# Optimization experiments

Hardware: AMD Instinct MI355X
Metric: run time of the kernel (lower is better)

The kernel has to match this reference:

```python
import jax, jax.numpy as jnp
import numpy as np

B, C, H, W, N, NH, DFF = 2, 256, 128, 128, 8, 8, 1024
EPS = 1e-5


def _ln(x, g, b):
    m = jnp.mean(x, -1, keepdims=True)
    v = jnp.mean((x - m) ** 2, -1, keepdims=True)
    return (x - m) / jnp.sqrt(v + EPS) * g + b


def _mha(q, k, v, Wqkv, bqkv, Wo, bo, nh):
    # q,k,v: [Bq, S, C]; torch MultiheadAttention with packed in_proj
    Bq, S, Cd = q.shape
    dh = Cd // nh
    Wq, Wk, Wv = jnp.split(Wqkv, 3, axis=0)
    bq, bk, bv = jnp.split(bqkv, 3, axis=0)
    qp = (q @ Wq.T + bq).reshape(Bq, S, nh, dh).transpose(0, 2, 1, 3)
    kp = (k @ Wk.T + bk).reshape(Bq, S, nh, dh).transpose(0, 2, 1, 3)
    vp = (v @ Wv.T + bv).reshape(Bq, S, nh, dh).transpose(0, 2, 1, 3)
    scores = jnp.einsum('bhqd,bhkd->bhqk', qp, kp) / jnp.sqrt(jnp.asarray(dh, qp.dtype))
    attn = jax.nn.softmax(scores, axis=-1)
    o = jnp.einsum('bhqk,bhkd->bhqd', attn, vp).transpose(0, 2, 1, 3).reshape(Bq, S, Cd)
    return o @ Wo.T + bo


def _enc_layer(q, k, v, Wqkv, bqkv, Wo, bo, W1, b1, W2, b2, g1, be1, g2, be2, nh):
    # normalize_before=False, dropout=0
    src = _ln(v + _mha(q, k, v, Wqkv, bqkv, Wo, bo, nh), g1, be1)
    ffn = jax.nn.relu(src @ W1.T + b1) @ W2.T + b2
    return _ln(src + ffn, g2, be2)


def _encode(feat, pe, layer_params, nh):
    # feat: [Nv, hw, C]; pe = glob_pos + rel_pos broadcast: [Nv, hw, C]
    out = feat
    qk = out + pe
    out = _enc_layer(qk, qk, out, *layer_params, nh)
    out_t = out.transpose(1, 0, 2)                 # [hw, Nv, C] axis-permuted pass
    qk = out_t + pe.transpose(1, 0, 2)
    out = _enc_layer(qk, qk, out_t, *layer_params, nh).transpose(1, 0, 2)
    return out


def _forward(backbone_memory, defe_feature_filtered, glob_pos_embed,
             Wqkv, bqkv, Wo, bo, W1, b1, W2, b2, g1, be1, g2, be2,
             relW1, relb1, relW2, relb2, n):
    Bm, Cd, Hf, Wf = backbone_memory.shape
    h, w = Hf // n, Wf // n
    Nv, hw = n * n, h * w

    # relative position embedding: MLP over normalized grid coords [h,w,2]
    gy, gx = jnp.meshgrid(jnp.arange(h, dtype=jnp.float32),
                          jnp.arange(w, dtype=jnp.float32), indexing='ij')
    coords = jnp.stack([gx / (w - 1), gy / (h - 1)], axis=-1)
    rel = (jax.nn.relu(coords @ relW1.T + relb1) @ relW2.T + relb2)  # [h,w,C]
    rel = rel.reshape(1, hw, Cd)                                      # [1,hw,C]

    # window partition: [B, Nv, hw, C]
    win = backbone_memory.reshape(Bm, Cd, n, h, n, w).transpose(0, 2, 4, 1, 3, 5)
    win = win.reshape(Bm, Nv, Cd, hw).transpose(0, 1, 3, 2)

    # per-window global pos embed: [Nv, hw, C]
    glob = glob_pos_embed.reshape(Cd, n, h, n, w).transpose(1, 3, 0, 2, 4)
    glob = glob.reshape(Nv, Cd, hw).transpose(0, 2, 1)

    pe = glob + rel
    layer_params = (Wqkv, bqkv, Wo, bo, W1, b1, W2, b2, g1, be1, g2, be2)
    enc = jax.vmap(lambda f: _encode(f, pe, layer_params, NH))(win)   # [B,Nv,hw,C]

    # scatter windows back and add residually (reconstructed += feats)
    back = enc.transpose(0, 1, 3, 2).reshape(Bm, n, n, Cd, h, w)
    back = back.transpose(0, 3, 1, 4, 2, 5).reshape(Bm, Cd, Hf, Wf)
    reconstructed = backbone_memory + back

    # defe_mask via non-overlapping max-pool (all-ones mask -> all valid)
    Hm, Wm = defe_feature_filtered.shape[-2:]
    kh = (Hm // Hf) * h
    kw = (Wm // Wf) * w
    pooled = defe_feature_filtered.reshape(Bm, 1, n, kh, n, kw).max(axis=(3, 5))
    defe_mask = pooled[:, 0] > 0
    return reconstructed, defe_mask


def setup_inputs() -> dict:
    key = jax.random.key(0)
    ks = jax.random.split(key, 10)
    s = 0.02
    return {
        'backbone_memory': jax.random.normal(ks[0], (B, C, H, W), jnp.float32),
        'defe_feature_filtered': jnp.ones((B, 1, H, W), jnp.float32),
        'glob_pos_embed': jax.random.normal(ks[1], (C, H, W), jnp.float32),
        'Wqkv': jax.random.normal(ks[2], (3 * C, C), jnp.float32) * s,
        'bqkv': jnp.zeros((3 * C,), jnp.float32),
        'Wo': jax.random.normal(ks[3], (C, C), jnp.float32) * s,
        'bo': jnp.zeros((C,), jnp.float32),
        'W1': jax.random.normal(ks[4], (DFF, C), jnp.float32) * s,
        'b1': jnp.zeros((DFF,), jnp.float32),
        'W2': jax.random.normal(ks[5], (C, DFF), jnp.float32) * s,
        'b2': jnp.zeros((C,), jnp.float32),
        'g1': jnp.ones((C,), jnp.float32),
        'be1': jnp.zeros((C,), jnp.float32),
        'g2': jnp.ones((C,), jnp.float32),
        'be2': jnp.zeros((C,), jnp.float32),
        'relW1': jax.random.normal(ks[6], (64, 2), jnp.float32) * s,
        'relb1': jnp.zeros((64,), jnp.float32),
        'relW2': jax.random.normal(ks[7], (C, 64), jnp.float32) * s,
        'relb2': jnp.zeros((C,), jnp.float32),
        'n': N,
    }


def reference(backbone_memory, defe_feature_filtered, glob_pos_embed,
              Wqkv, bqkv, Wo, bo, W1, b1, W2, b2, g1, be1, g2, be2,
              relW1, relb1, relW2, relb2, n):
    return _forward(backbone_memory, defe_feature_filtered, glob_pos_embed,
                    Wqkv, bqkv, Wo, bo, W1, b1, W2, b2, g1, be1, g2, be2,
                    relW1, relb1, relW2, relb2, n)
```

## Files before the change

### kernel.cpp

```cpp
#include <hip/hip_runtime.h>
#include <hip/hip_bf16.h>

#define C_DIM 256
#define NHEAD 8
#define DH 32
#define NTOK 32768
#define PETOK 16384
#define DFF_DIM 1024
#define LN_EPS 1e-5f

typedef unsigned int u32;
typedef unsigned short ushortT;
using frag_ab = __attribute__((ext_vector_type(8))) short;
using f32x4   = __attribute__((ext_vector_type(4))) float;

__device__ __forceinline__ float bflo(u32 u) { union { u32 i; float f; } c; c.i = u << 16; return c.f; }
__device__ __forceinline__ float bfhi(u32 u) { union { u32 i; float f; } c; c.i = u & 0xffff0000u; return c.f; }
__device__ __forceinline__ ushortT f2b(float f) {
    __hip_bfloat16 b = __float2bfloat16(f);
    return *reinterpret_cast<ushortT*>(&b);
}
__device__ __forceinline__ u32 packbf(float lo, float hi) {
    return (u32)f2b(lo) | ((u32)f2b(hi) << 16);
}
__device__ __forceinline__ void gload_lds16(const ushortT* g, ushortT* l) {
    __builtin_amdgcn_global_load_lds((const __attribute__((address_space(1))) void*)g,
                                     (__attribute__((address_space(3))) void*)l, 16, 0, 0);
}

__global__ void cvt_all_kernel(const float* __restrict__ Wqkv, const float* __restrict__ Wo,
                               const float* __restrict__ W1, const float* __restrict__ W2,
                               ushortT* __restrict__ dst) {
    const int i = (blockIdx.x * 256 + threadIdx.x) * 4;
    const float* src;
    int off;
    if (i < 196608)      { src = Wqkv; off = 0; }
    else if (i < 262144) { src = Wo;   off = 196608; }
    else if (i < 524288) { src = W1;   off = 262144; }
    else                 { src = W2;   off = 524288; }
    const float4 v = *(const float4*)&src[i - off];
    uint2 o = {packbf(v.x, v.y), packbf(v.z, v.w)};
    *(uint2*)&dst[i] = o;
}

__global__ void rel_kernel(const float* __restrict__ relW1, const float* __restrict__ relb1,
                           const float* __restrict__ relW2, const float* __restrict__ relb2,
                           float* __restrict__ rel) {
    __shared__ float hid[64];
    int t = blockIdx.x;
    int ty = t >> 4, tx = t & 15;
    float cx = tx * (1.0f / 15.0f);
    float cy = ty * (1.0f / 15.0f);
    int c = threadIdx.x;
    if (c < 64) {
        float h = relW1[c * 2 + 0] * cx + relW1[c * 2 + 1] * cy + relb1[c];
        hid[c] = fmaxf(h, 0.0f);
    }
    __syncthreads();
    float acc = relb2[c];
    #pragma unroll
    for (int jj = 0; jj < 64; ++jj) acc = fmaf(hid[jj], relW2[c * 64 + jj], acc);
    rel[t * C_DIM + c] = acc;
}

__global__ __launch_bounds__(256) void pe_kernel(const float* __restrict__ glob,
                                                 const float* __restrict__ rel,
                                                 ushortT* __restrict__ peb) {
    __shared__ float tile[32][129];
    const int y = blockIdx.x;
    const int c0 = blockIdx.y * 32;
    const int i = y >> 4, ty = y & 15;
    const int tid = threadIdx.x;
    const int xl = tid & 127;
    #pragma unroll
    for (int p = 0; p < 16; ++p) {
        const int cl = p * 2 + (tid >> 7);
        tile[cl][xl] = glob[(size_t)(c0 + cl) * 16384 + y * 128 + xl];
    }
    __syncthreads();
    const int cl = tid & 31;
    #pragma unroll
    for (int p = 0; p < 16; ++p) {
        const int x = p * 8 + (tid >> 5);
        const int v = i * 8 + (x >> 4);
        const int t = ty * 16 + (x & 15);
        const float val = tile[cl][x] + rel[t * C_DIM + c0 + cl];
        peb[(size_t)(v * 256 + t) * C_DIM + c0 + cl] = f2b(val);
    }
}

__global__ __launch_bounds__(256) void window_kernel(const float* __restrict__ backbone,
                                                     float* __restrict__ Xf, ushortT* __restrict__ Xb) {
    __shared__ float tile[32][129];
    const int y = blockIdx.x;
    const int c0 = blockIdx.y * 32;
    const int b = blockIdx.z;
    const int i = y >> 4, ty = y & 15;
    const int tid = threadIdx.x;
    const int xl = tid & 127;
    #pragma unroll
    for (int p = 0; p < 16; ++p) {
        const int cl = p * 2 + (tid >> 7);
        tile[cl][xl] = backbone[(size_t)b * 4194304 + (size_t)(c0 + cl) * 16384 + y * 128 + xl];
    }
    __syncthreads();
    const int cl = tid & 31;
    #pragma unroll
    for (int p = 0; p < 16; ++p) {
        const int x = p * 8 + (tid >> 5);
        const int v = i * 8 + (x >> 4);
        const int t = ty * 16 + (x & 15);
        const size_t tok = (size_t)b * PETOK + v * 256 + t;
        const float val = tile[cl][x];
        Xf[tok * C_DIM + c0 + cl] = val;
        Xb[tok * C_DIM + c0 + cl] = f2b(val);
    }
}

__global__ __launch_bounds__(256) void scatter_kernel(const float* __restrict__ backbone,
                                                      const float* __restrict__ X,
                                                      float* __restrict__ out) {
    __shared__ float tile[128][33];
    const int y = blockIdx.x;
    const int c0 = blockIdx.y * 32;
    const int b = blockIdx.z;
    const int i = y >> 4, ty = y & 15;
    const int tid = threadIdx.x;
    const int cl = tid & 31;
    #pragma unroll
    for (int p = 0; p < 16; ++p) {
        const int x = p * 8 + (tid >> 5);
        const int v = i * 8 + (x >> 4);
        const int t = ty * 16 + (x & 15);
        const size_t tok = (size_t)b * PETOK + v * 256 + t;
        tile[x][cl] = X[tok * C_DIM + c0 + cl];
    }
    __syncthreads();
    const int xl = tid & 127;
    #pragma unroll
    for (int p = 0; p < 16; ++p) {
        const int c = c0 + p * 2 + (tid >> 7);
        const size_t gi = (size_t)b * 4194304 + (size_t)c * 16384 + y * 128 + xl;
        out[gi] = backbone[gi] + tile[xl][p * 2 + (tid >> 7)];
    }
}

#define BM 128
#define BN 128
#define BK 32

template<bool FUSE_PE, bool RELU>
__global__ __launch_bounds__(256) void gemm_bf16(
        const ushortT* __restrict__ A, int lda,
        const ushortT* __restrict__ peb,
        const ushortT* __restrict__ W,
        const float* __restrict__ bias,
        ushortT* __restrict__ Cout, int ldc, int K) {
    __shared__ ushortT As[BM][BK];
    __shared__ ushortT Bs[BN][BK];
    const int m0 = blockIdx.y * BM;
    const int n0 = blockIdx.x * BN;
    const int tid = threadIdx.x;
    const int lane = tid & 63;
    const int wave = tid >> 6;
    const int wm = (wave >> 1) * 64;
    const int wn = (wave & 1) * 64;
    const int fr = lane & 15;
    const int fg = lane >> 4;
    const int gRow = wave * 32 + (lane >> 2);
    const int gCol = (lane & 3) * 8;
    const int sRow = tid >> 2;
    const int sCol = (tid & 3) * 8;

    f32x4 acc[4][4];
    #pragma unroll
    for (int i = 0; i < 4; ++i)
        #pragma unroll
        for (int j = 0; j < 4; ++j)
            acc[i][j] = (f32x4){0.f, 0.f, 0.f, 0.f};

    for (int k0 = 0; k0 < K; k0 += BK) {
        if (FUSE_PE) {
            #pragma unroll
            for (int h = 0; h < 2; ++h) {
                const int row = sRow + h * 64;
                uint4 av = *(const uint4*)&A[(size_t)(m0 + row) * lda + k0 + sCol];
                const uint4 pv = *(const uint4*)&peb[(size_t)((m0 + row) & 16383) * C_DIM + k0 + sCol];
                u32* a = (u32*)&av;
                const u32* p = (const u32*)&pv;
                #pragma unroll
                for (int e = 0; e < 4; ++e)
                    a[e] = packbf(bflo(a[e]) + bflo(p[e]), bfhi(a[e]) + bfhi(p[e]));
                *(uint4*)&As[row][sCol] = av;
            }
        } else {
            gload_lds16(&A[(size_t)(m0 + gRow) * lda + k0 + gCol], &As[wave * 32][0]);
            gload_lds16(&A[(size_t)(m0 + gRow + 16) * lda + k0 + gCol], &As[wave * 32 + 16][0]);
        }
        gload_lds16(&W[(size_t)(n0 + gRow) * K + k0 + gCol], &Bs[wave * 32][0]);
        gload_lds16(&W[(size_t)(n0 + gRow + 16) * K + k0 + gCol], &Bs[wave * 32 + 16][0]);
        __syncthreads();
        frag_ab af[4], bf[4];
        #pragma unroll
        for (int i = 0; i < 4; ++i) af[i] = *(const frag_ab*)&As[wm + i * 16 + fr][fg * 8];
        #pragma unroll
        for (int j = 0; j < 4; ++j) bf[j] = *(const frag_ab*)&Bs[wn + j * 16 + fr][fg * 8];
        #pragma unroll
        for (int i = 0; i < 4; ++i)
            #pragma unroll
            for (int j = 0; j < 4; ++j)
                acc[i][j] = __builtin_amdgcn_mfma_f32_16x16x32_bf16(af[i], bf[j], acc[i][j], 0, 0, 0);
        __syncthreads();
    }
    #pragma unroll
    for (int j = 0; j < 4; ++j) {
        const float bv = bias[n0 + wn + j * 16 + fr];
        #pragma unroll
        for (int i = 0; i < 4; ++i) {
            #pragma unroll
            for (int r = 0; r < 4; ++r) {
                float v = acc[i][j][r] + bv;
                if (RELU) v = fmaxf(v, 0.0f);
                const int m = m0 + wm + i * 16 + fg * 4 + r;
                const int n = n0 + wn + j * 16 + fr;
                Cout[(size_t)m * ldc + n] = f2b(v);
            }
        }
    }
}

#define KVC 128
__global__ __launch_bounds__(256) void attn_p0(const ushortT* __restrict__ QKb,
                                               const ushortT* __restrict__ Vb,
                                               ushortT* __restrict__ Ob) {
    __shared__ ushortT K_lds[KVC * 40];
    __shared__ ushortT V_t[32 * 136];
    __shared__ ushortT P_lds[4][16 * 136];
    const int grp = blockIdx.x;
    const int h = grp & 7;
    const int bv = grp >> 3;
    const int base = (bv >> 6) * PETOK + (bv & 63) * 256;
    const int tid = threadIdx.x;
    const int wave = tid >> 6;
    const int lane = tid & 63;
    const int fr = lane & 15;
    const int fg = lane >> 4;
    const float scale = 0.17677669529663687f;

    frag_ab qf[4];
    size_t qtok[4];
    #pragma unroll
    for (int s = 0; s < 4; ++s) {
        qtok[s] = (size_t)(base + wave * 64 + s * 16 + fr);
        qf[s] = *(const frag_ab*)&QKb[qtok[s] * 512 + h * DH + fg * 8];
    }
    float m[4], l[4];
    f32x4 o0[4], o1[4];
    #pragma unroll
    for (int s = 0; s < 4; ++s) {
        m[s] = -1e30f; l[s] = 0.f;
        o0[s] = (f32x4){0.f, 0.f, 0.f, 0.f};
        o1[s] = (f32x4){0.f, 0.f, 0.f, 0.f};
    }

    for (int c = 0; c < 2; ++c) {
        __syncthreads();
        #pragma unroll
        for (int it = 0; it < 2; ++it) {
            const int idx = it * 256 + tid;
            const int row = idx >> 2, ch = idx & 3;
            const size_t tok = (size_t)(base + c * KVC + row);
            const uint4 kv = *(const uint4*)&QKb[tok * 512 + 256 + h * DH + ch * 8];
            *(uint4*)&K_lds[row * 40 + ch * 8] = kv;
            const uint4 vv = *(const uint4*)&Vb[tok * C_DIM + h * DH + ch * 8];
            const ushortT* vp = (const ushortT*)&vv;
            #pragma unroll
            for (int e = 0; e < 8; ++e) V_t[(ch * 8 + e) * 136 + row] = vp[e];
        }
        __syncthreads();
        #pragma unroll
        for (int s = 0; s < 4; ++s) {
            f32x4 sc[8];
            #pragma unroll
            for (int kt = 0; kt < 8; ++kt) {
                const frag_ab kf = *(const frag_ab*)&K_lds[(kt * 16 + fr) * 40 + fg * 8];
                sc[kt] = __builtin_amdgcn_mfma_f32_16x16x32_bf16(kf, qf[s], (f32x4){0.f, 0.f, 0.f, 0.f}, 0, 0, 0);
            }
            float mx = -1e30f;
            #pragma unroll
            for (int kt = 0; kt < 8; ++kt)
                mx = fmaxf(mx, fmaxf(fmaxf(sc[kt][0], sc[kt][1]), fmaxf(sc[kt][2], sc[kt][3])));
            mx = fmaxf(mx, __shfl_xor(mx, 16, 64));
            mx = fmaxf(mx, __shfl_xor(mx, 32, 64));
            const float nm = fmaxf(m[s], mx);
            const float corr = __expf((m[s] - nm) * scale);
            m[s] = nm;
            float lsum = 0.f;
            #pragma unroll
            for (int kt = 0; kt < 8; ++kt) {
                const float p0 = __expf((sc[kt][0] - nm) * scale);
                const float p1 = __expf((sc[kt][1] - nm) * scale);
                const float p2 = __expf((sc[kt][2] - nm) * scale);
                const float p3 = __expf((sc[kt][3] - nm) * scale);
                lsum += (p0 + p1) + (p2 + p3);
                uint2 pk;
                pk.x = packbf(p0, p1);
                pk.y = packbf(p2, p3);
                *(uint2*)&P_lds[wave][fr * 136 + kt * 16 + fg * 4] = pk;
            }
            lsum += __shfl_xor(lsum, 16, 64);
            lsum += __shfl_xor(lsum, 32, 64);
            l[s] = l[s] * corr + lsum;
            o0[s] *= corr;
            o1[s] *= corr;
            #pragma unroll
            for (int kc = 0; kc < 4; ++kc) {
                const frag_ab pf = *(const frag_ab*)&P_lds[wave][fr * 136 + kc * 32 + fg * 8];
                const frag_ab v0 = *(const frag_ab*)&V_t[fr * 136 + kc * 32 + fg * 8];
                const frag_ab v1 = *(const frag_ab*)&V_t[(16 + fr) * 136 + kc * 32 + fg * 8];
                o0[s] = __builtin_amdgcn_mfma_f32_16x16x32_bf16(v0, pf, o0[s], 0, 0, 0);
                o1[s] = __builtin_amdgcn_mfma_f32_16x16x32_bf16(v1, pf, o1[s], 0, 0, 0);
            }
        }
    }
    #pragma unroll
    for (int s = 0; s < 4; ++s) {
        const float inv = 1.0f / l[s];
        ushortT* ob = &Ob[qtok[s] * C_DIM + h * DH];
        uint2 w0, w1;
        w0.x = packbf(o0[s][0] * inv, o0[s][1] * inv);
        w0.y = packbf(o0[s][2] * inv, o0[s][3] * inv);
        w1.x = packbf(o1[s][0] * inv, o1[s][1] * inv);
        w1.y = packbf(o1[s][2] * inv, o1[s][3] * inv);
        *(uint2*)&ob[fg * 4] = w0;
        *(uint2*)&ob[16 + fg * 4] = w1;
    }
}

template<int S, int LDK, int LDV, int LDP>
__device__ __forceinline__ void attn_wave_work(
        const ushortT* __restrict__ QKb, ushortT* __restrict__ Ob,
        const ushortT* __restrict__ K_lds, const ushortT* __restrict__ V_t,
        ushortT* __restrict__ P_lds,
        int base, int seqStride, int head, int q0base) {
    constexpr int NKT = S / 16;
    constexpr int NKC = S / 32;
    const int lane = threadIdx.x & 63;
    const int fr = lane & 15;
    const int fg = lane >> 4;
    const float scale = 0.17677669529663687f;
    #pragma unroll
    for (int s = 0; s < 4; ++s) {
        const int qq = q0base + s * 16 + fr;
        const size_t qtok = (size_t)(base + qq * seqStride);
        const frag_ab qf = *(const frag_ab*)&QKb[qtok * 512 + head * DH + fg * 8];
        f32x4 sc[NKT];
        #pragma unroll
        for (int kt = 0; kt < NKT; ++kt) {
            const frag_ab kf = *(const frag_ab*)&K_lds[(kt * 16 + fr) * LDK + fg * 8];
            sc[kt] = __builtin_amdgcn_mfma_f32_16x16x32_bf16(kf, qf, (f32x4){0.f, 0.f, 0.f, 0.f}, 0, 0, 0);
        }
        float mx = -1e30f;
        #pragma unroll
        for (int kt = 0; kt < NKT; ++kt)
            mx = fmaxf(mx, fmaxf(fmaxf(sc[kt][0], sc[kt][1]), fmaxf(sc[kt][2], sc[kt][3])));
        mx = fmaxf(mx, __shfl_xor(mx, 16, 64));
        mx = fmaxf(mx, __shfl_xor(mx, 32, 64));
        float lsum = 0.f;
        #pragma unroll
        for (int kt = 0; kt < NKT; ++kt) {
            const float p0 = __expf((sc[kt][0] - mx) * scale);
            const float p1 = __expf((sc[kt][1] - mx) * scale);
            const float p2 = __expf((sc[kt][2] - mx) * scale);
            const float p3 = __expf((sc[kt][3] - mx) * scale);
            lsum += (p0 + p1) + (p2 + p3);
            uint2 pk;
            pk.x = packbf(p0, p1);
            pk.y = packbf(p2, p3);
            *(uint2*)&P_lds[fr * LDP + kt * 16 + fg * 4] = pk;
        }
        lsum += __shfl_xor(lsum, 16, 64);
        lsum += __shfl_xor(lsum, 32, 64);
        f32x4 o0 = {0.f, 0.f, 0.f, 0.f}, o1 = {0.f, 0.f, 0.f, 0.f};
        #pragma unroll
        for (int kc = 0; kc < NKC; ++kc) {
            const frag_ab pf = *(const frag_ab*)&P_lds[fr * LDP + kc * 32 + fg * 8];
            const frag_ab v0 = *(const frag_ab*)&V_t[fr * LDV + kc * 32 + fg * 8];
            const frag_ab v1 = *(const frag_ab*)&V_t[(16 + fr) * LDV + kc * 32 + fg * 8];
            o0 = __builtin_amdgcn_mfma_f32_16x16x32_bf16(v0, pf, o0, 0, 0, 0);
            o1 = __builtin_amdgcn_mfma_f32_16x16x32_bf16(v1, pf, o1, 0, 0, 0);
        }
        const float inv = 1.0f / lsum;
        ushortT* ob = &Ob[qtok * C_DIM + head * DH];
        uint2 w0, w1;
        w0.x = packbf(o0[0] * inv, o0[1] * inv);
        w0.y = packbf(o0[2] * inv, o0[3] * inv);
        w1.x = packbf(o1[0] * inv, o1[1] * inv);
        w1.y = packbf(o1[2] * inv, o1[3] * inv);
        *(uint2*)&ob[fg * 4] = w0;
        *(uint2*)&ob[16 + fg * 4] = w1;
    }
}

__global__ __launch_bounds__(256) void attn_p1(const ushortT* __restrict__ QKb,
                                               const ushortT* __restrict__ Vb,
                                               ushortT* __restrict__ Ob) {
    __shared__ ushortT K_lds[4][64 * 40];
    __shared__ ushortT V_t[4][32 * 72];
    __shared__ ushortT P_lds[4][16 * 72];
    const int wave = threadIdx.x >> 6;
    const int lane = threadIdx.x & 63;
    const int unit = blockIdx.x * 4 + wave;
    const int h = unit & 7;
    const int g = unit >> 3;
    const int base = (g >> 8) * PETOK + (g & 255);
    #pragma unroll
    for (int it = 0; it < 4; ++it) {
        const int idx = it * 64 + lane;
        const int row = idx >> 2, ch = idx & 3;
        const size_t tok = (size_t)(base + row * 256);
        const uint4 kv = *(const uint4*)&QKb[tok * 512 + 256 + h * DH + ch * 8];
        *(uint4*)&K_lds[wave][row * 40 + ch * 8] = kv;
        const uint4 vv = *(const uint4*)&Vb[tok * C_DIM + h * DH + ch * 8];
        const ushortT* vp = (const ushortT*)&vv;
        #pragma unroll
        for (int e = 0; e < 8; ++e) V_t[wave][(ch * 8 + e) * 72 + row] = vp[e];
    }
    attn_wave_work<64, 40, 72, 72>(QKb, Ob, K_lds[wave], V_t[wave], P_lds[wave], base, 256, h, 0);
}

__global__ __launch_bounds__(256) void ln_kernel(float* __restrict__ X, const ushortT* __restrict__ Y,
                                                 const float* __restrict__ g, const float* __restrict__ be,
                                                 ushortT* __restrict__ Xb) {
    int tok = blockIdx.x * 4 + (threadIdx.x >> 6);
    int lane = threadIdx.x & 63;
    float4 x = *(float4*)&X[(size_t)tok * C_DIM + lane * 4];
    const uint2 yu = *(const uint2*)&Y[(size_t)tok * C_DIM + lane * 4];
    float v0 = x.x + bflo(yu.x), v1 = x.y + bfhi(yu.x);
    float v2 = x.z + bflo(yu.y), v3 = x.w + bfhi(yu.y);
    float s = v0 + v1 + v2 + v3;
    float ss = v0 * v0 + v1 * v1 + v2 * v2 + v3 * v3;
    #pragma unroll
    for (int off = 32; off; off >>= 1) {
        s += __shfl_xor(s, off, 64);
        ss += __shfl_xor(ss, off, 64);
    }
    float mean = s * (1.0f / 256.0f);
    float var = ss * (1.0f / 256.0f) - mean * mean;
    float inv = rsqrtf(var + LN_EPS);
    const float4 gv = *(const float4*)&g[lane * 4];
    const float4 bv = *(const float4*)&be[lane * 4];
    float o0 = (v0 - mean) * inv * gv.x + bv.x;
    float o1 = (v1 - mean) * inv * gv.y + bv.y;
    float o2 = (v2 - mean) * inv * gv.z + bv.z;
    float o3 = (v3 - mean) * inv * gv.w + bv.w;
    float4 of = {o0, o1, o2, o3};
    *(float4*)&X[(size_t)tok * C_DIM + lane * 4] = of;
    uint2 ob = {packbf(o0, o1), packbf(o2, o3)};
    *(uint2*)&Xb[(size_t)tok * C_DIM + lane * 4] = ob;
}

__global__ void mask_kernel(const float* __restrict__ defe, float* __restrict__ out) {
    __shared__ float wmax[4];
    const int idx = blockIdx.x;
    const int b = idx >> 6;
    const int ii = (idx >> 3) & 7;
    const int jj = idx & 7;
    const int t = threadIdx.x;
    const int y = t >> 4, xx = t & 15;
    float v = defe[b * 16384 + (ii * 16 + y) * 128 + jj * 16 + xx];
    #pragma unroll
    for (int off = 32; off; off >>= 1) v = fmaxf(v, __shfl_xor(v, off, 64));
    if ((t & 63) == 0) wmax[t >> 6] = v;
    __syncthreads();
    if (t == 0) {
        float mx = fmaxf(fmaxf(wmax[0], wmax[1]), fmaxf(wmax[2], wmax[3]));
        out[8388608 + idx] = (mx > 0.0f) ? 1.0f : 0.0f;
    }
}

extern "C" void kernel_launch(void* const* d_in, const int* in_sizes, int n_in,
                              void* d_out, int out_size, void* d_ws, size_t ws_size,
                              hipStream_t stream) {
    const float* backbone = (const float*)d_in[0];
    const float* defe     = (const float*)d_in[1];
    const float* glob     = (const float*)d_in[2];
    const float* Wqkv     = (const float*)d_in[3];
    const float* bqkv     = (const float*)d_in[4];
    const float* Wo       = (const float*)d_in[5];
    const float* bo       = (const float*)d_in[6];
    const float* W1       = (const float*)d_in[7];
    const float* b1       = (const float*)d_in[8];
    const float* W2       = (const float*)d_in[9];
    const float* b2       = (const float*)d_in[10];
    const float* g1       = (const float*)d_in[11];
    const float* be1      = (const float*)d_in[12];
    const float* g2       = (const float*)d_in[13];
    const float* be2      = (const float*)d_in[14];
    const float* relW1    = (const float*)d_in[15];
    const float* relb1    = (const float*)d_in[16];
    const float* relW2    = (const float*)d_in[17];
    const float* relb2    = (const float*)d_in[18];

    ushortT* peb    = (ushortT*)d_ws;
    ushortT* Wqkv_b = peb + 4194304;
    ushortT* Wo_b   = Wqkv_b + 196608;
    ushortT* W1_b   = Wo_b + 65536;
    ushortT* W2_b   = W1_b + 262144;
    ushortT* Xb     = W2_b + 262144;
    ushortT* QKb    = Xb + 8388608;
    ushortT* Vb     = QKb + 16777216;
    ushortT* Ob     = Vb + 8388608;
    ushortT* Hb     = QKb;
    ushortT* Yb     = Ob + 8388608;
    float*   Xf     = (float*)(Yb + 8388608);
    float*   relf   = Xf + 8388608;
    size_t needed = (size_t)((char*)(relf + 65536) - (char*)d_ws);
    if (ws_size < needed) return;

    cvt_all_kernel<<<768, 256, 0, stream>>>(Wqkv, Wo, W1, W2, Wqkv_b);
    rel_kernel<<<256, 256, 0, stream>>>(relW1, relb1, relW2, relb2, relf);
    pe_kernel<<<dim3(128, 8), 256, 0, stream>>>(glob, relf, peb);
    window_kernel<<<dim3(128, 8, 2), 256, 0, stream>>>(backbone, Xf, Xb);

    for (int pass = 0; pass < 2; ++pass) {
        gemm_bf16<true, false><<<dim3(512 / BN, NTOK / BM), 256, 0, stream>>>(
            Xb, C_DIM, peb, Wqkv_b, bqkv, QKb, 512, C_DIM);
        gemm_bf16<false, false><<<dim3(256 / BN, NTOK / BM), 256, 0, stream>>>(
            Xb, C_DIM, nullptr, Wqkv_b + 512 * 256, bqkv + 512, Vb, C_DIM, C_DIM);
        if (pass == 0) {
            attn_p0<<<128 * NHEAD, 256, 0, stream>>>(QKb, Vb, Ob);
        } else {
            attn_p1<<<4096 / 4, 256, 0, stream>>>(QKb, Vb, Ob);
        }
        gemm_bf16<false, false><<<dim3(256 / BN, NTOK / BM), 256, 0, stream>>>(
            Ob, C_DIM, nullptr, Wo_b, bo, Yb, C_DIM, C_DIM);
        ln_kernel<<<NTOK / 4, 256, 0, stream>>>(Xf, Yb, g1, be1, Xb);
        gemm_bf16<false, true><<<dim3(DFF_DIM / BN, NTOK / BM), 256, 0, stream>>>(
            Xb, C_DIM, nullptr, W1_b, b1, Hb, DFF_DIM, C_DIM);
        gemm_bf16<false, false><<<dim3(256 / BN, NTOK / BM), 256, 0, stream>>>(
            Hb, DFF_DIM, nullptr, W2_b, b2, Yb, C_DIM, DFF_DIM);
        ln_kernel<<<NTOK / 4, 256, 0, stream>>>(Xf, Yb, g2, be2, Xb);
    }

    scatter_kernel<<<dim3(128, 8, 2), 256, 0, stream>>>(backbone, Xf, (float*)d_out);
    mask_kernel<<<128, 256, 0, stream>>>(defe, (float*)d_out);
}
```

Baseline: 411.3 us.

## Double-buffer GEMM LDS tiles, drop fp32 residual copy, skew V transpose stores

The GEMM kernel now double-buffers its A/B LDS tiles, prefetching the next K slice (via registers for the PE-fused path) while MFMAs run on the current slice, and needs one barrier per iteration instead of two. The fp32 residual stream Xf is removed: LayerNorm, windowing and scatter read and write only the bf16 copy, which cuts memory traffic but stores the residual at lower precision. The V transpose stores in both attention kernels are rotated per chunk to reduce LDS bank conflicts.

```diff
diff --git a/kernel.cpp b/kernel.cpp
--- a/kernel.cpp
+++ b/kernel.cpp
@@ -16,6 +16,7 @@
 
 __device__ __forceinline__ float bflo(u32 u) { union { u32 i; float f; } c; c.i = u << 16; return c.f; }
 __device__ __forceinline__ float bfhi(u32 u) { union { u32 i; float f; } c; c.i = u & 0xffff0000u; return c.f; }
+__device__ __forceinline__ float b2f(ushortT u) { union { u32 i; float f; } c; c.i = ((u32)u) << 16; return c.f; }
 __device__ __forceinline__ ushortT f2b(float f) {
     __hip_bfloat16 b = __float2bfloat16(f);
     return *reinterpret_cast<ushortT*>(&b);
@@ -90,7 +91,7 @@
 }
 
 __global__ __launch_bounds__(256) void window_kernel(const float* __restrict__ backbone,
-                                                     float* __restrict__ Xf, ushortT* __restrict__ Xb) {
+                                                     ushortT* __restrict__ Xb) {
     __shared__ float tile[32][129];
     const int y = blockIdx.x;
     const int c0 = blockIdx.y * 32;
@@ -111,16 +112,14 @@
         const int v = i * 8 + (x >> 4);
         const int t = ty * 16 + (x & 15);
         const size_t tok = (size_t)b * PETOK + v * 256 + t;
-        const float val = tile[cl][x];
-        Xf[tok * C_DIM + c0 + cl] = val;
-        Xb[tok * C_DIM + c0 + cl] = f2b(val);
+        Xb[tok * C_DIM + c0 + cl] = f2b(tile[cl][x]);
     }
 }
 
 __global__ __launch_bounds__(256) void scatter_kernel(const float* __restrict__ backbone,
-                                                      const float* __restrict__ X,
+                                                      const ushortT* __restrict__ X,
                                                       float* __restrict__ out) {
-    __shared__ float tile[128][33];
+    __shared__ ushortT tile[128][34];
     const int y = blockIdx.x;
     const int c0 = blockIdx.y * 32;
     const int b = blockIdx.z;
@@ -141,7 +140,7 @@
     for (int p = 0; p < 16; ++p) {
         const int c = c0 + p * 2 + (tid >> 7);
         const size_t gi = (size_t)b * 4194304 + (size_t)c * 16384 + y * 128 + xl;
-        out[gi] = backbone[gi] + tile[xl][p * 2 + (tid >> 7)];
+        out[gi] = backbone[gi] + b2f(tile[xl][p * 2 + (tid >> 7)]);
     }
 }
 
@@ -156,8 +155,8 @@
         const ushortT* __restrict__ W,
         const float* __restrict__ bias,
         ushortT* __restrict__ Cout, int ldc, int K) {
-    __shared__ ushortT As[BM][BK];
-    __shared__ ushortT Bs[BN][BK];
+    __shared__ ushortT As[2][BM][BK];
+    __shared__ ushortT Bs[2][BN][BK];
     const int m0 = blockIdx.y * BM;
     const int n0 = blockIdx.x * BN;
     const int tid = threadIdx.x;
@@ -171,6 +170,7 @@
     const int gCol = (lane & 3) * 8;
     const int sRow = tid >> 2;
     const int sCol = (tid & 3) * 8;
+    const int nk = K / BK;
 
     f32x4 acc[4][4];
     #pragma unroll
@@ -179,38 +179,77 @@
         for (int j = 0; j < 4; ++j)
             acc[i][j] = (f32x4){0.f, 0.f, 0.f, 0.f};
 
-    for (int k0 = 0; k0 < K; k0 += BK) {
-        if (FUSE_PE) {
-            #pragma unroll
-            for (int h = 0; h < 2; ++h) {
-                const int row = sRow + h * 64;
-                uint4 av = *(const uint4*)&A[(size_t)(m0 + row) * lda + k0 + sCol];
-                const uint4 pv = *(const uint4*)&peb[(size_t)((m0 + row) & 16383) * C_DIM + k0 + sCol];
-                u32* a = (u32*)&av;
-                const u32* p = (const u32*)&pv;
-                #pragma unroll
-                for (int e = 0; e < 4; ++e)
-                    a[e] = packbf(bflo(a[e]) + bflo(p[e]), bfhi(a[e]) + bfhi(p[e]));
-                *(uint4*)&As[row][sCol] = av;
-            }
-        } else {
-            gload_lds16(&A[(size_t)(m0 + gRow) * lda + k0 + gCol], &As[wave * 32][0]);
-            gload_lds16(&A[(size_t)(m0 + gRow + 16) * lda + k0 + gCol], &As[wave * 32 + 16][0]);
-        }
-        gload_lds16(&W[(size_t)(n0 + gRow) * K + k0 + gCol], &Bs[wave * 32][0]);
-        gload_lds16(&W[(size_t)(n0 + gRow + 16) * K + k0 + gCol], &Bs[wave * 32 + 16][0]);
-        __syncthreads();
+    uint4 avr0, avr1, pvr0, pvr1;
+    if (FUSE_PE) {
+        avr0 = *(const uint4*)&A[(size_t)(m0 + sRow) * lda + sCol];
+        pvr0 = *(const uint4*)&peb[(size_t)((m0 + sRow) & 16383) * C_DIM + sCol];
+        avr1 = *(const uint4*)&A[(size_t)(m0 + sRow + 64) * lda + sCol];
+        pvr1 = *(const uint4*)&peb[(size_t)((m0 + sRow + 64) & 16383) * C_DIM + sCol];
+        {
+            uint4 av = avr0; const uint4 pv = pvr0;
+            u32* a = (u32*)&av; const u32* p = (const u32*)&pv;
+            #pragma unroll
+            for (int e = 0; e < 4; ++e) a[e] = packbf(bflo(a[e]) + bflo(p[e]), bfhi(a[e]) + bfhi(p[e]));
+            *(uint4*)&As[0][sRow][sCol] = av;
+        }
+        {
+            uint4 av = avr1; const uint4 pv = pvr1;
+            u32* a = (u32*)&av; const u32* p = (const u32*)&pv;
+            #pragma unroll
+            for (int e = 0; e < 4; ++e) a[e] = packbf(bflo(a[e]) + bflo(p[e]), bfhi(a[e]) + bfhi(p[e]));
+            *(uint4*)&As[0][sRow + 64][sCol] = av;
+        }
+    } else {
+        gload_lds16(&A[(size_t)(m0 + gRow) * lda + gCol], &As[0][wave * 32][0]);
+        gload_lds16(&A[(size_t)(m0 + gRow + 16) * lda + gCol], &As[0][wave * 32 + 16][0]);
+    }
+    gload_lds16(&W[(size_t)(n0 + gRow) * K + gCol], &Bs[0][wave * 32][0]);
+    gload_lds16(&W[(size_t)(n0 + gRow + 16) * K + gCol], &Bs[0][wave * 32 + 16][0]);
+    __syncthreads();
+
+    int cur = 0;
+    for (int t = 0; t < nk; ++t) {
+        const int k1 = (t + 1) * BK;
+        const int nxt = cur ^ 1;
+        if (t + 1 < nk) {
+            if (FUSE_PE) {
+                avr0 = *(const uint4*)&A[(size_t)(m0 + sRow) * lda + k1 + sCol];
+                pvr0 = *(const uint4*)&peb[(size_t)((m0 + sRow) & 16383) * C_DIM + k1 + sCol];
+                avr1 = *(const uint4*)&A[(size_t)(m0 + sRow + 64) * lda + k1 + sCol];
+                pvr1 = *(const uint4*)&peb[(size_t)((m0 + sRow + 64) & 16383) * C_DIM + k1 + sCol];
+            } else {
+                gload_lds16(&A[(size_t)(m0 + gRow) * lda + k1 + gCol], &As[nxt][wave * 32][0]);
+                gload_lds16(&A[(size_t)(m0 + gRow + 16) * lda + k1 + gCol], &As[nxt][wave * 32 + 16][0]);
+            }
+            gload_lds16(&W[(size_t)(n0 + gRow) * K + k1 + gCol], &Bs[nxt][wave * 32][0]);
+            gload_lds16(&W[(size_t)(n0 + gRow + 16) * K + k1 + gCol], &Bs[nxt][wave * 32 + 16][0]);
+        }
         frag_ab af[4], bf[4];
         #pragma unroll
-        for (int i = 0; i < 4; ++i) af[i] = *(const frag_ab*)&As[wm + i * 16 + fr][fg * 8];
-        #pragma unroll
-        for (int j = 0; j < 4; ++j) bf[j] = *(const frag_ab*)&Bs[wn + j * 16 + fr][fg * 8];
+        for (int i = 0; i < 4; ++i) af[i] = *(const frag_ab*)&As[cur][wm + i * 16 + fr][fg * 8];
+        #pragma unroll
+        for (int j = 0; j < 4; ++j) bf[j] = *(const frag_ab*)&Bs[cur][wn + j * 16 + fr][fg * 8];
         #pragma unroll
         for (int i = 0; i < 4; ++i)
             #pragma unroll
             for (int j = 0; j < 4; ++j)
                 acc[i][j] = __builtin_amdgcn_mfma_f32_16x16x32_bf16(af[i], bf[j], acc[i][j], 0, 0, 0);
-        __syncthreads();
+        if (t + 1 < nk) {
+            if (FUSE_PE) {
+                uint4 av = avr0; const uint4 pv = pvr0;
+                u32* a = (u32*)&av; const u32* p = (const u32*)&pv;
+                #pragma unroll
+                for (int e = 0; e < 4; ++e) a[e] = packbf(bflo(a[e]) + bflo(p[e]), bfhi(a[e]) + bfhi(p[e]));
+                *(uint4*)&As[nxt][sRow][sCol] = av;
+                uint4 av2 = avr1; const uint4 pv2 = pvr1;
+                u32* a2 = (u32*)&av2; const u32* p2 = (const u32*)&pv2;
+                #pragma unroll
+                for (int e = 0; e < 4; ++e) a2[e] = packbf(bflo(a2[e]) + bflo(p2[e]), bfhi(a2[e]) + bfhi(p2[e]));
+                *(uint4*)&As[nxt][sRow + 64][sCol] = av2;
+            }
+            __syncthreads();
+        }
+        cur = nxt;
     }
     #pragma unroll
     for (int j = 0; j < 4; ++j) {
@@ -275,7 +314,10 @@
             const uint4 vv = *(const uint4*)&Vb[tok * C_DIM + h * DH + ch * 8];
             const ushortT* vp = (const ushortT*)&vv;
             #pragma unroll
-            for (int e = 0; e < 8; ++e) V_t[(ch * 8 + e) * 136 + row] = vp[e];
+            for (int e = 0; e < 8; ++e) {
+                const int dl = (e + 2 * ch) & 7;
+                V_t[(ch * 8 + dl) * 136 + row] = vp[dl];
+            }
         }
         __syncthreads();
         #pragma unroll
@@ -424,20 +466,22 @@
         const uint4 vv = *(const uint4*)&Vb[tok * C_DIM + h * DH + ch * 8];
         const ushortT* vp = (const ushortT*)&vv;
         #pragma unroll
-        for (int e = 0; e < 8; ++e) V_t[wave][(ch * 8 + e) * 72 + row] = vp[e];
+        for (int e = 0; e < 8; ++e) {
+            const int dl = (e + 2 * ch) & 7;
+            V_t[wave][(ch * 8 + dl) * 72 + row] = vp[dl];
+        }
     }
     attn_wave_work<64, 40, 72, 72>(QKb, Ob, K_lds[wave], V_t[wave], P_lds[wave], base, 256, h, 0);
 }
 
-__global__ __launch_bounds__(256) void ln_kernel(float* __restrict__ X, const ushortT* __restrict__ Y,
-                                                 const float* __restrict__ g, const float* __restrict__ be,
-                                                 ushortT* __restrict__ Xb) {
+__global__ __launch_bounds__(256) void ln_kernel(ushortT* __restrict__ X, const ushortT* __restrict__ Y,
+                                                 const float* __restrict__ g, const float* __restrict__ be) {
     int tok = blockIdx.x * 4 + (threadIdx.x >> 6);
     int lane = threadIdx.x & 63;
-    float4 x = *(float4*)&X[(size_t)tok * C_DIM + lane * 4];
+    const uint2 xu = *(const uint2*)&X[(size_t)tok * C_DIM + lane * 4];
     const uint2 yu = *(const uint2*)&Y[(size_t)tok * C_DIM + lane * 4];
-    float v0 = x.x + bflo(yu.x), v1 = x.y + bfhi(yu.x);
-    float v2 = x.z + bflo(yu.y), v3 = x.w + bfhi(yu.y);
+    float v0 = bflo(xu.x) + bflo(yu.x), v1 = bfhi(xu.x) + bfhi(yu.x);
+    float v2 = bflo(xu.y) + bflo(yu.y), v3 = bfhi(xu.y) + bfhi(yu.y);
     float s = v0 + v1 + v2 + v3;
     float ss = v0 * v0 + v1 * v1 + v2 * v2 + v3 * v3;
     #pragma unroll
@@ -454,10 +498,8 @@
     float o1 = (v1 - mean) * inv * gv.y + bv.y;
     float o2 = (v2 - mean) * inv * gv.z + bv.z;
     float o3 = (v3 - mean) * inv * gv.w + bv.w;
-    float4 of = {o0, o1, o2, o3};
-    *(float4*)&X[(size_t)tok * C_DIM + lane * 4] = of;
     uint2 ob = {packbf(o0, o1), packbf(o2, o3)};
-    *(uint2*)&Xb[(size_t)tok * C_DIM + lane * 4] = ob;
+    *(uint2*)&X[(size_t)tok * C_DIM + lane * 4] = ob;
 }
 
 __global__ void mask_kernel(const float* __restrict__ defe, float* __restrict__ out) {
@@ -513,15 +555,14 @@
     ushortT* Ob     = Vb + 8388608;
     ushortT* Hb     = QKb;
     ushortT* Yb     = Ob + 8388608;
-    float*   Xf     = (float*)(Yb + 8388608);
-    float*   relf   = Xf + 8388608;
+    float*   relf   = (float*)(Yb + 8388608);
     size_t needed = (size_t)((char*)(relf + 65536) - (char*)d_ws);
     if (ws_size < needed) return;
 
     cvt_all_kernel<<<768, 256, 0, stream>>>(Wqkv, Wo, W1, W2, Wqkv_b);
     rel_kernel<<<256, 256, 0, stream>>>(relW1, relb1, relW2, relb2, relf);
     pe_kernel<<<dim3(128, 8), 256, 0, stream>>>(glob, relf, peb);
-    window_kernel<<<dim3(128, 8, 2), 256, 0, stream>>>(backbone, Xf, Xb);
+    window_kernel<<<dim3(128, 8, 2), 256, 0, stream>>>(backbone, Xb);
 
     for (int pass = 0; pass < 2; ++pass) {
         gemm_bf16<true, false><<<dim3(512 / BN, NTOK / BM), 256, 0, stream>>>(
@@ -535,14 +576,14 @@
         }
         gemm_bf16<false, false><<<dim3(256 / BN, NTOK / BM), 256, 0, stream>>>(
             Ob, C_DIM, nullptr, Wo_b, bo, Yb, C_DIM, C_DIM);
-        ln_kernel<<<NTOK / 4, 256, 0, stream>>>(Xf, Yb, g1, be1, Xb);
+        ln_kernel<<<NTOK / 4, 256, 0, stream>>>(Xb, Yb, g1, be1);
         gemm_bf16<false, true><<<dim3(DFF_DIM / BN, NTOK / BM), 256, 0, stream>>>(
             Xb, C_DIM, nullptr, W1_b, b1, Hb, DFF_DIM, C_DIM);
         gemm_bf16<false, false><<<dim3(256 / BN, NTOK / BM), 256, 0, stream>>>(
             Hb, DFF_DIM, nullptr, W2_b, b2, Yb, C_DIM, DFF_DIM);
-        ln_kernel<<<NTOK / 4, 256, 0, stream>>>(Xf, Yb, g2, be2, Xb);
-    }
-
-    scatter_kernel<<<dim3(128, 8, 2), 256, 0, stream>>>(backbone, Xf, (float*)d_out);
+        ln_kernel<<<NTOK / 4, 256, 0, stream>>>(Xb, Yb, g2, be2);
+    }
+
+    scatter_kernel<<<dim3(128, 8, 2), 256, 0, stream>>>(backbone, Xb, (float*)d_out);
     mask_kernel<<<128, 256, 0, stream>>>(defe, (float*)d_out);
 }
```

After: 426.1 us. +3.6%, slower.

## Drop fp32 residual copy, keep residual in bf16, swizzle GEMM tile order

Applied to the files above, without the earlier changes.

The fp32 residual stream buffer is removed. Window, layer-norm and scatter kernels now read and write only the bf16 activation buffer, which cuts global memory traffic in these bandwidth-bound kernels. GEMM workgroups are remapped with an interleaved swizzle of the flat block index, meant to improve cache locality (the stride of 8 may map to XCDs). The attention helper is also inlined into attn_p1. Keeping the residual in bf16 lowers accuracy across the residual adds and layer norms.

```diff
diff --git a/kernel.cpp b/kernel.cpp
--- a/kernel.cpp
+++ b/kernel.cpp
@@ -16,6 +16,7 @@
 
 __device__ __forceinline__ float bflo(u32 u) { union { u32 i; float f; } c; c.i = u << 16; return c.f; }
 __device__ __forceinline__ float bfhi(u32 u) { union { u32 i; float f; } c; c.i = u & 0xffff0000u; return c.f; }
+__device__ __forceinline__ float b2f(ushortT u) { union { u32 i; float f; } c; c.i = ((u32)u) << 16; return c.f; }
 __device__ __forceinline__ ushortT f2b(float f) {
     __hip_bfloat16 b = __float2bfloat16(f);
     return *reinterpret_cast<ushortT*>(&b);
@@ -90,7 +91,7 @@
 }
 
 __global__ __launch_bounds__(256) void window_kernel(const float* __restrict__ backbone,
-                                                     float* __restrict__ Xf, ushortT* __restrict__ Xb) {
+                                                     ushortT* __restrict__ Xb) {
     __shared__ float tile[32][129];
     const int y = blockIdx.x;
     const int c0 = blockIdx.y * 32;
@@ -111,16 +112,14 @@
         const int v = i * 8 + (x >> 4);
         const int t = ty * 16 + (x & 15);
         const size_t tok = (size_t)b * PETOK + v * 256 + t;
-        const float val = tile[cl][x];
-        Xf[tok * C_DIM + c0 + cl] = val;
-        Xb[tok * C_DIM + c0 + cl] = f2b(val);
+        Xb[tok * C_DIM + c0 + cl] = f2b(tile[cl][x]);
     }
 }
 
 __global__ __launch_bounds__(256) void scatter_kernel(const float* __restrict__ backbone,
-                                                      const float* __restrict__ X,
+                                                      const ushortT* __restrict__ X,
                                                       float* __restrict__ out) {
-    __shared__ float tile[128][33];
+    __shared__ ushortT tile[128][34];
     const int y = blockIdx.x;
     const int c0 = blockIdx.y * 32;
     const int b = blockIdx.z;
@@ -141,7 +140,7 @@
     for (int p = 0; p < 16; ++p) {
         const int c = c0 + p * 2 + (tid >> 7);
         const size_t gi = (size_t)b * 4194304 + (size_t)c * 16384 + y * 128 + xl;
-        out[gi] = backbone[gi] + tile[xl][p * 2 + (tid >> 7)];
+        out[gi] = backbone[gi] + b2f(tile[xl][p * 2 + (tid >> 7)]);
     }
 }
 
@@ -158,8 +157,12 @@
         ushortT* __restrict__ Cout, int ldc, int K) {
     __shared__ ushortT As[BM][BK];
     __shared__ ushortT Bs[BN][BK];
-    const int m0 = blockIdx.y * BM;
-    const int n0 = blockIdx.x * BN;
+    const int nwg = gridDim.x * gridDim.y;
+    const int flat = blockIdx.y * gridDim.x + blockIdx.x;
+    const int cpx = nwg >> 3;
+    const int swz = (flat & 7) * cpx + (flat >> 3);
+    const int m0 = (swz / gridDim.x) * BM;
+    const int n0 = (swz % gridDim.x) * BN;
     const int tid = threadIdx.x;
     const int lane = tid & 63;
     const int wave = tid >> 6;
@@ -337,71 +340,6 @@
     }
 }
 
-template<int S, int LDK, int LDV, int LDP>
-__device__ __forceinline__ void attn_wave_work(
-        const ushortT* __restrict__ QKb, ushortT* __restrict__ Ob,
-        const ushortT* __restrict__ K_lds, const ushortT* __restrict__ V_t,
-        ushortT* __restrict__ P_lds,
-        int base, int seqStride, int head, int q0base) {
-    constexpr int NKT = S / 16;
-    constexpr int NKC = S / 32;
-    const int lane = threadIdx.x & 63;
-    const int fr = lane & 15;
-    const int fg = lane >> 4;
-    const float scale = 0.17677669529663687f;
-    #pragma unroll
-    for (int s = 0; s < 4; ++s) {
-        const int qq = q0base + s * 16 + fr;
-        const size_t qtok = (size_t)(base + qq * seqStride);
-        const frag_ab qf = *(const frag_ab*)&QKb[qtok * 512 + head * DH + fg * 8];
-        f32x4 sc[NKT];
-        #pragma unroll
-        for (int kt = 0; kt < NKT; ++kt) {
-            const frag_ab kf = *(const frag_ab*)&K_lds[(kt * 16 + fr) * LDK + fg * 8];
-            sc[kt] = __builtin_amdgcn_mfma_f32_16x16x32_bf16(kf, qf, (f32x4){0.f, 0.f, 0.f, 0.f}, 0, 0, 0);
-        }
-        float mx = -1e30f;
-        #pragma unroll
-        for (int kt = 0; kt < NKT; ++kt)
-            mx = fmaxf(mx, fmaxf(fmaxf(sc[kt][0], sc[kt][1]), fmaxf(sc[kt][2], sc[kt][3])));
-        mx = fmaxf(mx, __shfl_xor(mx, 16, 64));
-        mx = fmaxf(mx, __shfl_xor(mx, 32, 64));
-        float lsum = 0.f;
-        #pragma unroll
-        for (int kt = 0; kt < NKT; ++kt) {
-            const float p0 = __expf((sc[kt][0] - mx) * scale);
-            const float p1 = __expf((sc[kt][1] - mx) * scale);
-            const float p2 = __expf((sc[kt][2] - mx) * scale);
-            const float p3 = __expf((sc[kt][3] - mx) * scale);
-            lsum += (p0 + p1) + (p2 + p3);
-            uint2 pk;
-            pk.x = packbf(p0, p1);
-            pk.y = packbf(p2, p3);
-            *(uint2*)&P_lds[fr * LDP + kt * 16 + fg * 4] = pk;
-        }
-        lsum += __shfl_xor(lsum, 16, 64);
-        lsum += __shfl_xor(lsum, 32, 64);
-        f32x4 o0 = {0.f, 0.f, 0.f, 0.f}, o1 = {0.f, 0.f, 0.f, 0.f};
-        #pragma unroll
-        for (int kc = 0; kc < NKC; ++kc) {
-            const frag_ab pf = *(const frag_ab*)&P_lds[fr * LDP + kc * 32 + fg * 8];
-            const frag_ab v0 = *(const frag_ab*)&V_t[fr * LDV + kc * 32 + fg * 8];
-            const frag_ab v1 = *(const frag_ab*)&V_t[(16 + fr) * LDV + kc * 32 + fg * 8];
-            o0 = __builtin_amdgcn_mfma_f32_16x16x32_bf16(v0, pf, o0, 0, 0, 0);
-            o1 = __builtin_amdgcn_mfma_f32_16x16x32_bf16(v1, pf, o1, 0, 0, 0);
-        }
-        const float inv = 1.0f / lsum;
-        ushortT* ob = &Ob[qtok * C_DIM + head * DH];
-        uint2 w0, w1;
-        w0.x = packbf(o0[0] * inv, o0[1] * inv);
-        w0.y = packbf(o0[2] * inv, o0[3] * inv);
-        w1.x = packbf(o1[0] * inv, o1[1] * inv);
-        w1.y = packbf(o1[2] * inv, o1[3] * inv);
-        *(uint2*)&ob[fg * 4] = w0;
-        *(uint2*)&ob[16 + fg * 4] = w1;
-    }
-}
-
 __global__ __launch_bounds__(256) void attn_p1(const ushortT* __restrict__ QKb,
                                                const ushortT* __restrict__ Vb,
                                                ushortT* __restrict__ Ob) {
@@ -414,6 +352,9 @@
     const int h = unit & 7;
     const int g = unit >> 3;
     const int base = (g >> 8) * PETOK + (g & 255);
+    const int fr = lane & 15;
+    const int fg = lane >> 4;
+    const float scale = 0.17677669529663687f;
     #pragma unroll
     for (int it = 0; it < 4; ++it) {
         const int idx = it * 64 + lane;
@@ -426,18 +367,67 @@
         #pragma unroll
         for (int e = 0; e < 8; ++e) V_t[wave][(ch * 8 + e) * 72 + row] = vp[e];
     }
-    attn_wave_work<64, 40, 72, 72>(QKb, Ob, K_lds[wave], V_t[wave], P_lds[wave], base, 256, h, 0);
-}
-
-__global__ __launch_bounds__(256) void ln_kernel(float* __restrict__ X, const ushortT* __restrict__ Y,
-                                                 const float* __restrict__ g, const float* __restrict__ be,
-                                                 ushortT* __restrict__ Xb) {
+    #pragma unroll
+    for (int s = 0; s < 4; ++s) {
+        const int qq = s * 16 + fr;
+        const size_t qtok = (size_t)(base + qq * 256);
+        const frag_ab qf = *(const frag_ab*)&QKb[qtok * 512 + h * DH + fg * 8];
+        f32x4 sc[4];
+        #pragma unroll
+        for (int kt = 0; kt < 4; ++kt) {
+            const frag_ab kf = *(const frag_ab*)&K_lds[wave][(kt * 16 + fr) * 40 + fg * 8];
+            sc[kt] = __builtin_amdgcn_mfma_f32_16x16x32_bf16(kf, qf, (f32x4){0.f, 0.f, 0.f, 0.f}, 0, 0, 0);
+        }
+        float mx = -1e30f;
+        #pragma unroll
+        for (int kt = 0; kt < 4; ++kt)
+            mx = fmaxf(mx, fmaxf(fmaxf(sc[kt][0], sc[kt][1]), fmaxf(sc[kt][2], sc[kt][3])));
+        mx = fmaxf(mx, __shfl_xor(mx, 16, 64));
+        mx = fmaxf(mx, __shfl_xor(mx, 32, 64));
+        float lsum = 0.f;
+        #pragma unroll
+        for (int kt = 0; kt < 4; ++kt) {
+            const float p0 = __expf((sc[kt][0] - mx) * scale);
+            const float p1 = __expf((sc[kt][1] - mx) * scale);
+            const float p2 = __expf((sc[kt][2] - mx) * scale);
+            const float p3 = __expf((sc[kt][3] - mx) * scale);
+            lsum += (p0 + p1) + (p2 + p3);
+            uint2 pk;
+            pk.x = packbf(p0, p1);
+            pk.y = packbf(p2, p3);
+            *(uint2*)&P_lds[wave][fr * 72 + kt * 16 + fg * 4] = pk;
+        }
+        lsum += __shfl_xor(lsum, 16, 64);
+        lsum += __shfl_xor(lsum, 32, 64);
+        f32x4 o0 = {0.f, 0.f, 0.f, 0.f}, o1 = {0.f, 0.f, 0.f, 0.f};
+        #pragma unroll
+        for (int kc = 0; kc < 2; ++kc) {
+            const frag_ab pf = *(const frag_ab*)&P_lds[wave][fr * 72 + kc * 32 + fg * 8];
+            const frag_ab v0 = *(const frag_ab*)&V_t[wave][fr * 72 + kc * 32 + fg * 8];
+            const frag_ab v1 = *(const frag_ab*)&V_t[wave][(16 + fr) * 72 + kc * 32 + fg * 8];
+            o0 = __builtin_amdgcn_mfma_f32_16x16x32_bf16(v0, pf, o0, 0, 0, 0);
+            o1 = __builtin_amdgcn_mfma_f32_16x16x32_bf16(v1, pf, o1, 0, 0, 0);
+        }
+        const float inv = 1.0f / lsum;
+        ushortT* ob = &Ob[qtok * C_DIM + h * DH];
+        uint2 w0, w1;
+        w0.x = packbf(o0[0] * inv, o0[1] * inv);
+        w0.y = packbf(o0[2] * inv, o0[3] * inv);
+        w1.x = packbf(o1[0] * inv, o1[1] * inv);
+        w1.y = packbf(o1[2] * inv, o1[3] * inv);
+        *(uint2*)&ob[fg * 4] = w0;
+        *(uint2*)&ob[16 + fg * 4] = w1;
+    }
+}
+
+__global__ __launch_bounds__(256) void ln_kernel(ushortT* __restrict__ X, const ushortT* __restrict__ Y,
+                                                 const float* __restrict__ g, const float* __restrict__ be) {
     int tok = blockIdx.x * 4 + (threadIdx.x >> 6);
     int lane = threadIdx.x & 63;
-    float4 x = *(float4*)&X[(size_t)tok * C_DIM + lane * 4];
+    const uint2 xu = *(const uint2*)&X[(size_t)tok * C_DIM + lane * 4];
     const uint2 yu = *(const uint2*)&Y[(size_t)tok * C_DIM + lane * 4];
-    float v0 = x.x + bflo(yu.x), v1 = x.y + bfhi(yu.x);
-    float v2 = x.z + bflo(yu.y), v3 = x.w + bfhi(yu.y);
+    float v0 = bflo(xu.x) + bflo(yu.x), v1 = bfhi(xu.x) + bfhi(yu.x);
+    float v2 = bflo(xu.y) + bflo(yu.y), v3 = bfhi(xu.y) + bfhi(yu.y);
     float s = v0 + v1 + v2 + v3;
     float ss = v0 * v0 + v1 * v1 + v2 * v2 + v3 * v3;
     #pragma unroll
@@ -454,10 +444,8 @@
     float o1 = (v1 - mean) * inv * gv.y + bv.y;
     float o2 = (v2 - mean) * inv * gv.z + bv.z;
     float o3 = (v3 - mean) * inv * gv.w + bv.w;
-    float4 of = {o0, o1, o2, o3};
-    *(float4*)&X[(size_t)tok * C_DIM + lane * 4] = of;
     uint2 ob = {packbf(o0, o1), packbf(o2, o3)};
-    *(uint2*)&Xb[(size_t)tok * C_DIM + lane * 4] = ob;
+    *(uint2*)&X[(size_t)tok * C_DIM + lane * 4] = ob;
 }
 
 __global__ void mask_kernel(const float* __restrict__ defe, float* __restrict__ out) {
@@ -513,15 +501,14 @@
     ushortT* Ob     = Vb + 8388608;
     ushortT* Hb     = QKb;
     ushortT* Yb     = Ob + 8388608;
-    float*   Xf     = (float*)(Yb + 8388608);
-    float*   relf   = Xf + 8388608;
+    float*   relf   = (float*)(Yb + 8388608);
     size_t needed = (size_t)((char*)(relf + 65536) - (char*)d_ws);
     if (ws_size < needed) return;
 
     cvt_all_kernel<<<768, 256, 0, stream>>>(Wqkv, Wo, W1, W2, Wqkv_b);
     rel_kernel<<<256, 256, 0, stream>>>(relW1, relb1, relW2, relb2, relf);
     pe_kernel<<<dim3(128, 8), 256, 0, stream>>>(glob, relf, peb);
-    window_kernel<<<dim3(128, 8, 2), 256, 0, stream>>>(backbone, Xf, Xb);
+    window_kernel<<<dim3(128, 8, 2), 256, 0, stream>>>(backbone, Xb);
 
     for (int pass = 0; pass < 2; ++pass) {
         gemm_bf16<true, false><<<dim3(512 / BN, NTOK / BM), 256, 0, stream>>>(
@@ -535,14 +522,14 @@
         }
         gemm_bf16<false, false><<<dim3(256 / BN, NTOK / BM), 256, 0, stream>>>(
             Ob, C_DIM, nullptr, Wo_b, bo, Yb, C_DIM, C_DIM);
-        ln_kernel<<<NTOK / 4, 256, 0, stream>>>(Xf, Yb, g1, be1, Xb);
+        ln_kernel<<<NTOK / 4, 256, 0, stream>>>(Xb, Yb, g1, be1);
         gemm_bf16<false, true><<<dim3(DFF_DIM / BN, NTOK / BM), 256, 0, stream>>>(
             Xb, C_DIM, nullptr, W1_b, b1, Hb, DFF_DIM, C_DIM);
         gemm_bf16<false, false><<<dim3(256 / BN, NTOK / BM), 256, 0, stream>>>(
             Hb, DFF_DIM, nullptr, W2_b, b2, Yb, C_DIM, DFF_DIM);
-        ln_kernel<<<NTOK / 4, 256, 0, stream>>>(Xf, Yb, g2, be2, Xb);
-    }
-
-    scatter_kernel<<<dim3(128, 8, 2), 256, 0, stream>>>(backbone, Xf, (float*)d_out);
+        ln_kernel<<<NTOK / 4, 256, 0, stream>>>(Xb, Yb, g2, be2);
+    }
+
+    scatter_kernel<<<dim3(128, 8, 2), 256, 0, stream>>>(backbone, Xb, (float*)d_out);
     mask_kernel<<<128, 256, 0, stream>>>(defe, (float*)d_out);
 }
```

New measurement: 352.5 us. -14.3%, faster.
